# Kernel tuning notes

Measured on AMD Instinct MI355X. Metric: run time of the kernel, lower is better.

## Reference

```python
import jax, jax.numpy as jnp
import numpy as np

B, L, C, H = 8, 2048, 512, 8
HD = C // H
MLP_H = int(C * 4.0)
LN_EPS = 1e-5


def _dwconv(x, w, b, groups):
    # x: (B, C, L), w: (C, C//groups, 3), 'same' padding depthwise/grouped conv
    y = jax.lax.conv_general_dilated(
        x, w, window_strides=(1,), padding=((1, 1),),
        feature_group_count=groups,
        dimension_numbers=('NCH', 'OIH', 'NCH'))
    return y + b[None, :, None]


def _ln(x, g, b):
    mu = x.mean(-1, keepdims=True)
    var = ((x - mu) ** 2).mean(-1, keepdims=True)
    return (x - mu) * jax.lax.rsqrt(var + LN_EPS) * g + b


def setup_inputs() -> dict:
    key = jax.random.key(0)
    ks = jax.random.split(key, 32)
    s = 0.02
    d = {
        'x_q': jax.random.normal(ks[0], (B, L, C), jnp.float32),
        'x_kv': jax.random.normal(ks[1], (B, L, C), jnp.float32),
        'cpe1_w': jax.random.normal(ks[2], (C, 1, 3), jnp.float32) * s,
        'cpe1_b': jnp.zeros((C,), jnp.float32),
        'norm1_g': jnp.ones((C,), jnp.float32),
        'norm1_b': jnp.zeros((C,), jnp.float32),
        'in_w': jax.random.normal(ks[3], (C, C), jnp.float32) * s,
        'in_b': jnp.zeros((C,), jnp.float32),
        'act_w': jax.random.normal(ks[4], (C, C), jnp.float32) * s,
        'act_b': jnp.zeros((C,), jnp.float32),
        'dwc_w': jax.random.normal(ks[5], (C, 1, 3), jnp.float32) * s,
        'dwc_b': jnp.zeros((C,), jnp.float32),
        'q_w': jax.random.normal(ks[6], (C, C), jnp.float32) * s,
        'q_b': jnp.zeros((C,), jnp.float32),
        'kv_w': jax.random.normal(ks[7], (C, 2 * C), jnp.float32) * s,
        'kv_b': jnp.zeros((2 * C,), jnp.float32),
        'lepe_w': jax.random.normal(ks[8], (C, 1, 3), jnp.float32) * s,
        'lepe_b': jnp.zeros((C,), jnp.float32),
        'out_w': jax.random.normal(ks[9], (C, C), jnp.float32) * s,
        'out_b': jnp.zeros((C,), jnp.float32),
        'cpe2_w': jax.random.normal(ks[10], (C, 1, 3), jnp.float32) * s,
        'cpe2_b': jnp.zeros((C,), jnp.float32),
        'norm2_g': jnp.ones((C,), jnp.float32),
        'norm2_b': jnp.zeros((C,), jnp.float32),
        'fc1_w': jax.random.normal(ks[11], (C, MLP_H), jnp.float32) * s,
        'fc1_b': jnp.zeros((MLP_H,), jnp.float32),
        'fc2_w': jax.random.normal(ks[12], (MLP_H, C), jnp.float32) * s,
        'fc2_b': jnp.zeros((C,), jnp.float32),
    }
    return d


def _linear_attention(x_q, x_kv, q_w, q_b, kv_w, kv_b, lepe_w, lepe_b):
    b, n, c = x_kv.shape
    kv = x_kv @ kv_w + kv_b                       # (b, n, 2c)
    k, v = kv[..., :c], kv[..., c:]
    q = jax.nn.elu(x_q @ q_w + q_b) + 1.0
    k = jax.nn.elu(k) + 1.0
    # (b, h, n, d)
    q = q.reshape(b, n, H, HD).transpose(0, 2, 1, 3)
    k = k.reshape(b, n, H, HD).transpose(0, 2, 1, 3)
    v = v.reshape(b, n, H, HD).transpose(0, 2, 1, 3)
    k_mean = k.mean(axis=2)                       # (b, h, d)
    z = 1.0 / (jnp.einsum('bhnd,bhd->bhn', q, k_mean) + 1e-6)
    scale = n ** (-0.5)
    kv_mat = jnp.einsum('bhnd,bhne->bhde', k * scale, v * scale)  # (b,h,d,d)
    out = jnp.einsum('bhnd,bhde->bhne', q, kv_mat) * z[..., None]
    out = out.transpose(0, 2, 1, 3).reshape(b, n, c)
    v_flat = v.transpose(0, 2, 1, 3).reshape(b, n, c).transpose(0, 2, 1)  # (b,c,n)
    out = out + _dwconv(v_flat, lepe_w, lepe_b, groups=c).transpose(0, 2, 1)
    return out


def reference(x_q, x_kv, cpe1_w, cpe1_b, norm1_g, norm1_b, in_w, in_b, act_w,
              act_b, dwc_w, dwc_b, q_w, q_b, kv_w, kv_b, lepe_w, lepe_b,
              out_w, out_b, cpe2_w, cpe2_b, norm2_g, norm2_b, fc1_w, fc1_b,
              fc2_w, fc2_b):
    b, l, c = x_kv.shape
    x = x_kv + _dwconv(x_kv.transpose(0, 2, 1), cpe1_w, cpe1_b, c).transpose(0, 2, 1)
    shortcut = x
    x = _ln(x, norm1_g, norm1_b)
    act_res = jax.nn.silu(x @ act_w + act_b)
    # NOTE: torch uses .view(B, C, L): a reshape, not a transpose -- replicate faithfully
    xp = (x @ in_w + in_b).reshape(b, c, l)
    xp = jax.nn.silu(_dwconv(xp, dwc_w, dwc_b, c)).reshape(b, l, c)
    xa = _linear_attention(x_q, xp, q_w, q_b, kv_w, kv_b, lepe_w, lepe_b)
    x = shortcut + ((xa * act_res) @ out_w + out_b)
    x = x + _dwconv(x.transpose(0, 2, 1), cpe2_w, cpe2_b, c).transpose(0, 2, 1)
    h = _ln(x, norm2_g, norm2_b)
    h = jax.nn.gelu(h @ fc1_w + fc1_b, approximate=False) @ fc2_w + fc2_b
    return x + h
```

## Files before the change

### kernel.cpp

```cpp
#include <hip/hip_runtime.h>
#include <cmath>


typedef __bf16 bf16;
typedef __bf16 bf16x8 __attribute__((ext_vector_type(8)));
typedef __bf16 bf16x4 __attribute__((ext_vector_type(4)));
typedef float  f32x4  __attribute__((ext_vector_type(4)));

#define B_  8
#define L_  2048
#define C_  512
#define M_  (B_ * L_)

__device__ __forceinline__ float fastrcp(float x) { return __builtin_amdgcn_rcpf(x); }

__device__ __forceinline__ float siluf(float x)
{
    return x * fastrcp(1.f + __expf(-x));
}
__device__ __forceinline__ float elu1f(float x) { return x > 0.f ? x + 1.f : __expf(x); }

__device__ __forceinline__ float geluf(float x)
{
    const float z = fabsf(x) * 0.70710678118654752f;
    const float t = fastrcp(__builtin_fmaf(z, 0.47047f, 1.f));
    const float poly = t * (0.3480242f + t * (-0.0958798f + t * 0.7478556f));
    const float erfz = __builtin_fmaf(-poly, __expf(-z * z), 1.f);
    const float hx = 0.5f * x;
    return __builtin_fmaf(hx, __builtin_copysignf(erfz, x), hx);
}

__device__ __forceinline__ void load_lds16(const bf16* g, bf16* l)
{
    __builtin_amdgcn_global_load_lds(
        (const __attribute__((address_space(1))) void*)g,
        (__attribute__((address_space(3))) void*)l, 16, 0, 0);
}

__global__ __launch_bounds__(256) void zero_k(float* __restrict__ p, int n)
{
    int i = blockIdx.x * 256 + threadIdx.x;
    if (i < n) p[i] = 0.f;
}

__global__ __launch_bounds__(64) void ws_diag_k(float* __restrict__ out, float v)
{
    if (threadIdx.x == 0 && blockIdx.x == 0) out[0] = v;
}

__global__ __launch_bounds__(256) void f32_to_bf16_k(
    const float* __restrict__ in, bf16* __restrict__ out, int n4)
{
    int i = blockIdx.x * 256 + threadIdx.x;
    if (i >= n4) return;
    float4 v = ((const float4*)in)[i];
    bf16x4 o = { (bf16)v.x, (bf16)v.y, (bf16)v.z, (bf16)v.w };
    ((bf16x4*)out)[i] = o;
}

struct TJob  { const float* W; bf16* Wt; int K; int N; int blk0; };
struct TJobs { TJob j[7]; };

__global__ __launch_bounds__(256) void transpose_all_k(TJobs jobs)
{
    __shared__ float tile[32][33];
    const int bid = blockIdx.x;
    int ji = 0;
#pragma unroll
    for (int i = 1; i < 7; ++i) if (bid >= jobs.j[i].blk0) ji = i;
    const float* W  = jobs.j[ji].W;
    bf16*        Wt = jobs.j[ji].Wt;
    const int K = jobs.j[ji].K, N = jobs.j[ji].N;
    const int rel = bid - jobs.j[ji].blk0;
    const int nb = N >> 5;
    const int n0 = (rel % nb) * 32, k0 = (rel / nb) * 32;
    const int tx = threadIdx.x & 31, ty = threadIdx.x >> 5;
#pragma unroll
    for (int i = 0; i < 32; i += 8)
        tile[ty + i][tx] = W[(size_t)(k0 + ty + i) * N + n0 + tx];
    __syncthreads();
#pragma unroll
    for (int i = 0; i < 32; i += 8)
        Wt[(size_t)(n0 + ty + i) * K + k0 + tx] = (bf16)tile[tx][ty + i];
}

__global__ __launch_bounds__(256) void cpe_ln_k(
    const float* __restrict__ xin, const float* __restrict__ cw,
    const float* __restrict__ cb, const float* __restrict__ g,
    const float* __restrict__ bb, float* __restrict__ xres,
    bf16* __restrict__ xln)
{
    const int token = blockIdx.x;
    const int l = token & (L_ - 1);
    const int tid = threadIdx.x;
    const float* row = xin + (size_t)token * C_;
    float v[2]; float s = 0.f, s2 = 0.f;
#pragma unroll
    for (int i = 0; i < 2; ++i) {
        const int c = tid + i * 256;
        float x0 = row[c];
        float xm = (l > 0)      ? row[c - C_] : 0.f;
        float xp = (l < L_ - 1) ? row[c + C_] : 0.f;
        float t = x0 + xm * cw[3*c] + x0 * cw[3*c+1] + xp * cw[3*c+2] + cb[c];
        v[i] = t; s += t; s2 += t * t;
    }
#pragma unroll
    for (int off = 32; off; off >>= 1) { s += __shfl_down(s, off); s2 += __shfl_down(s2, off); }
    __shared__ float rs[4], rs2[4];
    if ((tid & 63) == 0) { rs[tid >> 6] = s; rs2[tid >> 6] = s2; }
    __syncthreads();
    s  = rs[0] + rs[1] + rs[2] + rs[3];
    s2 = rs2[0] + rs2[1] + rs2[2] + rs2[3];
    const float mu = s * (1.f / C_);
    const float rstd = rsqrtf(s2 * (1.f / C_) - mu * mu + 1e-5f);
    float* orow = xres + (size_t)token * C_;
    bf16*  lrow = xln  + (size_t)token * C_;
#pragma unroll
    for (int i = 0; i < 2; ++i) {
        const int c = tid + i * 256;
        orow[c] = v[i];
        lrow[c] = (bf16)((v[i] - mu) * rstd * g[c] + bb[c]);
    }
}

__global__ __launch_bounds__(256) void dwc_silu_k(
    const bf16* __restrict__ Y, const float* __restrict__ w,
    const float* __restrict__ b, bf16* __restrict__ xp)
{
    const size_t idx = (size_t)blockIdx.x * 256 + threadIdx.x;
    const int m = (int)(idx & (size_t)(L_ * C_ - 1));
    const int ch = m >> 11;
    const int pos = m & (L_ - 1);
    float x0 = (float)Y[idx];
    float xm = (pos > 0)      ? (float)Y[idx - 1] : 0.f;
    float xq = (pos < L_ - 1) ? (float)Y[idx + 1] : 0.f;
    float t = xm * w[3*ch] + x0 * w[3*ch+1] + xq * w[3*ch+2] + b[ch];
    xp[idx] = (bf16)siluf(t);
}

__global__ __launch_bounds__(256) void ksum_k(
    const bf16* __restrict__ kvbT, float* __restrict__ ksum)
{
    const int c = blockIdx.x;
    const int wave = threadIdx.x >> 6, lane = threadIdx.x & 63;
#pragma unroll
    for (int i = 0; i < 2; ++i) {
        const int b = wave + i * 4;
        const bf16* src = kvbT + (size_t)c * M_ + b * L_ + lane * 32;
        float s = 0.f;
#pragma unroll
        for (int u = 0; u < 4; ++u) {
            bf16x8 v = *(const bf16x8*)(src + u * 8);
#pragma unroll
            for (int j = 0; j < 8; ++j) s += (float)v[j];
        }
#pragma unroll
        for (int o = 32; o; o >>= 1) s += __shfl_down(s, o);
        if (lane == 0) ksum[b * C_ + c] = s;
    }
}

__global__ __launch_bounds__(256) void kvmat_mfma_k(
    const bf16* __restrict__ kvbT, float* __restrict__ kvpart)
{
    const int bh = blockIdx.x, b = bh >> 3, h = bh & 7;
    const int tid = threadIdx.x;
    const int wave = tid >> 6, lane = tid & 63;
    const int l16 = lane & 15, quad = lane >> 4;
    __shared__ bf16 As[64 * 72];
    __shared__ bf16 Bs[64 * 72];
    const int r = tid >> 2;
    const int cseg = (tid & 3) * 16;
    const size_t kRow = (size_t)(h * 64 + r) * M_;
    const size_t vRow = (size_t)(512 + h * 64 + r) * M_;

    f32x4 acc[4];
    const f32x4 z4 = { 0.f, 0.f, 0.f, 0.f };
#pragma unroll
    for (int ni = 0; ni < 4; ++ni) acc[ni] = z4;

    for (int it = 0; it < 8; ++it) {
        const size_t colBase = (size_t)b * L_ + blockIdx.y * 512 + it * 64;
        {
            const bf16* ga = kvbT + vRow + colBase + cseg;
            const bf16* gb = kvbT + kRow + colBase + cseg;
            *(uint4*)&As[r * 72 + cseg]     = *(const uint4*)ga;
            *(uint4*)&As[r * 72 + cseg + 8] = *(const uint4*)(ga + 8);
            *(uint4*)&Bs[r * 72 + cseg]     = *(const uint4*)gb;
            *(uint4*)&Bs[r * 72 + cseg + 8] = *(const uint4*)(gb + 8);
        }
        __syncthreads();
#pragma unroll
        for (int kk = 0; kk < 64; kk += 32) {
            bf16x8 af = *(const bf16x8*)(&As[(wave * 16 + l16) * 72 + kk + quad * 8]);
#pragma unroll
            for (int ni = 0; ni < 4; ++ni) {
                bf16x8 bfr = *(const bf16x8*)(&Bs[(ni * 16 + l16) * 72 + kk + quad * 8]);
                acc[ni] = __builtin_amdgcn_mfma_f32_16x16x32_bf16(af, bfr, acc[ni], 0, 0, 0);
            }
        }
        __syncthreads();
    }
    float* dst = kvpart + (size_t)blockIdx.y * 262144 + (size_t)bh * 4096;
#pragma unroll
    for (int ni = 0; ni < 4; ++ni)
#pragma unroll
        for (int rr = 0; rr < 4; ++rr)
            dst[(wave * 16 + quad * 4 + rr) * 64 + ni * 16 + l16] = acc[ni][rr];
}

__global__ __launch_bounds__(256) void kvconv_k(
    const float* __restrict__ p, bf16* __restrict__ out)
{
    int i = blockIdx.x * 256 + threadIdx.x;
    float s = p[i] + p[i + 262144] + p[i + 2 * 262144] + p[i + 3 * 262144];
    out[i] = (bf16)(s * (1.f / (float)L_));
}

__global__ __launch_bounds__(256) void attn_mfma_k(
    const bf16* __restrict__ q, const bf16* __restrict__ kvbT,
    const bf16* __restrict__ kvmatT, const float* __restrict__ ksum,
    const float* __restrict__ lw, const float* __restrict__ lb,
    const bf16* __restrict__ act_res, bf16* __restrict__ xa_mul)
{
    const int bh = blockIdx.x, b = bh >> 3, h = bh & 7;
    const int n0 = blockIdx.y * 64;
    const int tid = threadIdx.x;
    const int wave = tid >> 6, lane = tid & 63;
    const int l16 = lane & 15, quad = lane >> 4;

    __shared__ bf16 kvT[64 * 72];
    __shared__ bf16 kmS[64];

#pragma unroll
    for (int i = 0; i < 2; ++i) {
        const int idx = i * 256 + tid;
        const int row = idx >> 3, col = (idx & 7) * 8;
        *(bf16x8*)&kvT[row * 72 + col] =
            *(const bf16x8*)&kvmatT[(size_t)bh * 4096 + idx * 8];
    }
    if (tid < 64) kmS[tid] = (bf16)(ksum[b * C_ + h * 64 + tid] * (1.f / (float)L_));
    __syncthreads();

    const int tok = n0 + wave * 16;
    const bf16* qbase = q + ((size_t)b * L_ + tok) * C_ + h * 64;
    const bf16x8 af0 = *(const bf16x8*)(qbase + (size_t)l16 * C_ + quad * 8);
    const bf16x8 af1 = *(const bf16x8*)(qbase + (size_t)l16 * C_ + 32 + quad * 8);

    const bf16x8 z8 = { bf16(0.f), bf16(0.f), bf16(0.f), bf16(0.f),
                        bf16(0.f), bf16(0.f), bf16(0.f), bf16(0.f) };
    const bf16x8 km0 = *(const bf16x8*)&kmS[quad * 8];
    const bf16x8 km1 = *(const bf16x8*)&kmS[32 + quad * 8];
    const bf16x8 b20 = (l16 == 0) ? km0 : z8;
    const bf16x8 b21 = (l16 == 0) ? km1 : z8;
    f32x4 zd = { 0.f, 0.f, 0.f, 0.f };
    zd = __builtin_amdgcn_mfma_f32_16x16x32_bf16(af0, b20, zd, 0, 0, 0);
    zd = __builtin_amdgcn_mfma_f32_16x16x32_bf16(af1, b21, zd, 0, 0, 0);
    float zr[4];
#pragma unroll
    for (int r = 0; r < 4; ++r)
        zr[r] = fastrcp(__shfl(zd[r], (lane & 48)) + 1e-6f);

    f32x4 acc[4];
    const f32x4 zf4 = { 0.f, 0.f, 0.f, 0.f };
#pragma unroll
    for (int ni = 0; ni < 4; ++ni) acc[ni] = zf4;
#pragma unroll
    for (int ni = 0; ni < 4; ++ni) {
        const bf16x8 b0 = *(const bf16x8*)&kvT[(ni * 16 + l16) * 72 + quad * 8];
        const bf16x8 b1 = *(const bf16x8*)&kvT[(ni * 16 + l16) * 72 + 32 + quad * 8];
        acc[ni] = __builtin_amdgcn_mfma_f32_16x16x32_bf16(af0, b0, acc[ni], 0, 0, 0);
        acc[ni] = __builtin_amdgcn_mfma_f32_16x16x32_bf16(af1, b1, acc[ni], 0, 0, 0);
    }

#pragma unroll
    for (int ni = 0; ni < 4; ++ni) {
        const int e = ni * 16 + l16;
        const int c = h * 64 + e;
        const float w0 = lw[3*c], w1 = lw[3*c+1], w2 = lw[3*c+2], lbc = lb[c];
        const bf16* vrow = kvbT + (size_t)(512 + c) * M_ + b * L_;
#pragma unroll
        for (int r = 0; r < 4; ++r) {
            const int n = tok + quad * 4 + r;
            const float v0 = (float)vrow[n];
            const float vm = (n > 0)      ? (float)vrow[n - 1] : 0.f;
            const float vp = (n < L_ - 1) ? (float)vrow[n + 1] : 0.f;
            const float lepe = vm * w0 + v0 * w1 + vp * w2 + lbc;
            const float xa = acc[ni][r] * zr[r] + lepe;
            const size_t off = ((size_t)b * L_ + n) * C_ + c;
            xa_mul[off] = (bf16)(xa * (float)act_res[off]);
        }
    }
}

template <int EPI>
__global__ __launch_bounds__(256) void gemm_bt(
    const bf16* __restrict__ A, const bf16* __restrict__ Bt,
    const float* __restrict__ bias, const float* __restrict__ res,
    void* __restrict__ outp, void* __restrict__ outp2, int K, int N)
{
    __shared__ bf16 As[128 * 64];
    __shared__ bf16 Bs[128 * 64];
    const int tid = threadIdx.x;
    const int wave = tid >> 6, lane = tid & 63;
    const int wm = (wave & 1) * 64, wn = (wave >> 1) * 64;
    const int l16 = lane & 15, quad = lane >> 4;
    const size_t tileM = (size_t)blockIdx.x * 128;
    const size_t tileN = (size_t)blockIdx.y * 128;

    const int lrow = lane >> 3;
    const int lcol = (((lane & 7) ^ (lrow & 7))) * 8;
    const int swz  = l16 & 7;

    const f32x4 z4 = { 0.f, 0.f, 0.f, 0.f };
    f32x4 acc[4][4];
#pragma unroll
    for (int mi = 0; mi < 4; ++mi)
#pragma unroll
        for (int ni = 0; ni < 4; ++ni) acc[mi][ni] = z4;

    for (int k0 = 0; k0 < K; k0 += 64) {
#pragma unroll
        for (int it = 0; it < 4; ++it) {
            const int rg = it * 32 + wave * 8;
            load_lds16(A  + (tileM + rg + lrow) * (size_t)K + k0 + lcol, As + rg * 64);
            load_lds16(Bt + (tileN + rg + lrow) * (size_t)K + k0 + lcol, Bs + rg * 64);
        }
        __syncthreads();
#pragma unroll
        for (int kk = 0; kk < 64; kk += 32) {
            bf16x8 af[4], bfr[4];
#pragma unroll
            for (int mi = 0; mi < 4; ++mi)
                af[mi] = *(const bf16x8*)(&As[(wm + mi * 16 + l16) * 64
                                              + ((((kk >> 3) + quad) ^ swz) * 8)]);
#pragma unroll
            for (int ni = 0; ni < 4; ++ni)
                bfr[ni] = *(const bf16x8*)(&Bs[(wn + ni * 16 + l16) * 64
                                               + ((((kk >> 3) + quad) ^ swz) * 8)]);
#pragma unroll
            for (int mi = 0; mi < 4; ++mi)
#pragma unroll
                for (int ni = 0; ni < 4; ++ni)
                    acc[mi][ni] = __builtin_amdgcn_mfma_f32_16x16x32_bf16(
                        af[mi], bfr[ni], acc[mi][ni], 0, 0, 0);
        }
        __syncthreads();
    }

#pragma unroll
    for (int mi = 0; mi < 4; ++mi) {
#pragma unroll
        for (int ni = 0; ni < 4; ++ni) {
#pragma unroll
            for (int r = 0; r < 4; ++r) {
                const size_t row = tileM + wm + mi * 16 + quad * 4 + r;
                const int   col = (int)tileN + wn + ni * 16 + l16;
                float v = acc[mi][ni][r];
                const size_t oidx = row * (size_t)N + col;
                if (EPI == 2)      ((bf16*)outp)[oidx] = (bf16)elu1f(v + bias[col]);
                else if (EPI == 4) ((bf16*)outp)[oidx] = (bf16)geluf(v + bias[col]);
                else if (EPI == 5) ((float*)outp)[oidx] = v + bias[col] + res[oidx];
                else if (EPI == 7) {
                    v += bias[(int)row];
                    ((bf16*)outp)[oidx] = (bf16)((row < 512) ? elu1f(v) : v);
                } else if (EPI == 8) {
                    const size_t orow = row * (size_t)512;
                    if (col < 512) ((bf16*)outp )[orow + col]       = (bf16)siluf(v + bias[col]);
                    else           ((bf16*)outp2)[orow + col - 512] = (bf16)(v + res[col - 512]);
                }
            }
        }
    }
}

#define OFF_WT_ACTIN ((size_t)0)
#define OFF_WT_Q    ((size_t)1048576)
#define OFF_WT_KV   ((size_t)1572864)
#define OFF_WT_OUT  ((size_t)2621440)
#define OFF_WT_FC1  ((size_t)3145728)
#define OFF_WT_FC2  ((size_t)5242880)
#define OFF_XLN     ((size_t)7340032)
#define OFF_ACTRES  ((size_t)24117248)
#define OFF_Y       ((size_t)40894464)
#define OFF_XP      ((size_t)57671680)
#define OFF_KV      ((size_t)74448896)
#define OFF_KSUM    ((size_t)108003328)
#define OFF_XAMUL   ((size_t)109068288)
#define OFF_X3      ((size_t)24117248)
#define OFF_H1      ((size_t)57671680)
#define WS_REQUIRED ((size_t)125845504)

extern "C" void kernel_launch(void* const* d_in, const int* in_sizes, int n_in,
                              void* d_out, int out_size, void* d_ws, size_t ws_size,
                              hipStream_t stream)
{
    const float* x_q    = (const float*)d_in[0];
    const float* x_kv   = (const float*)d_in[1];
    const float* cpe1_w = (const float*)d_in[2];
    const float* cpe1_b = (const float*)d_in[3];
    const float* n1_g   = (const float*)d_in[4];
    const float* n1_b   = (const float*)d_in[5];
    const float* in_w   = (const float*)d_in[6];
    const float* in_b   = (const float*)d_in[7];
    const float* act_w  = (const float*)d_in[8];
    const float* act_b  = (const float*)d_in[9];
    const float* dwc_w  = (const float*)d_in[10];
    const float* dwc_b  = (const float*)d_in[11];
    const float* q_w    = (const float*)d_in[12];
    const float* q_b    = (const float*)d_in[13];
    const float* kv_w   = (const float*)d_in[14];
    const float* kv_b   = (const float*)d_in[15];
    const float* lepe_w = (const float*)d_in[16];
    const float* lepe_b = (const float*)d_in[17];
    const float* out_w  = (const float*)d_in[18];
    const float* out_b  = (const float*)d_in[19];
    const float* cpe2_w = (const float*)d_in[20];
    const float* cpe2_b = (const float*)d_in[21];
    const float* n2_g   = (const float*)d_in[22];
    const float* n2_b   = (const float*)d_in[23];
    const float* fc1_w  = (const float*)d_in[24];
    const float* fc1_b  = (const float*)d_in[25];
    const float* fc2_w  = (const float*)d_in[26];
    const float* fc2_b  = (const float*)d_in[27];

    float* outf = (float*)d_out;

    if (ws_size < WS_REQUIRED) {
        zero_k<<<(out_size + 255) / 256, 256, 0, stream>>>(outf, out_size);
        ws_diag_k<<<1, 64, 0, stream>>>(outf, (float)ws_size);
        return;
    }

    char* ws = (char*)d_ws;
    bf16*  wt_actin = (bf16*)(ws + OFF_WT_ACTIN);
    bf16*  wt_q   = (bf16*)(ws + OFF_WT_Q);
    bf16*  wt_kv  = (bf16*)(ws + OFF_WT_KV);
    bf16*  wt_out = (bf16*)(ws + OFF_WT_OUT);
    bf16*  wt_fc1 = (bf16*)(ws + OFF_WT_FC1);
    bf16*  wt_fc2 = (bf16*)(ws + OFF_WT_FC2);
    bf16*  xln    = (bf16*)(ws + OFF_XLN);
    bf16*  xqb    = (bf16*)(ws + OFF_XLN);
    bf16*  kvbf   = (bf16*)(ws + OFF_XLN);
    bf16*  hln    = (bf16*)(ws + OFF_XLN);
    bf16*  actres = (bf16*)(ws + OFF_ACTRES);
    bf16*  Y      = (bf16*)(ws + OFF_Y);
    bf16*  qb     = (bf16*)(ws + OFF_Y);
    bf16*  xp     = (bf16*)(ws + OFF_XP);
    float* kvpart = (float*)(ws + OFF_XP);
    bf16*  kvbT   = (bf16*)(ws + OFF_KV);
    float* ksum   = (float*)(ws + OFF_KSUM);
    bf16*  xamul  = (bf16*)(ws + OFF_XAMUL);
    float* x3     = (float*)(ws + OFF_X3);
    bf16*  h1     = (bf16*)(ws + OFF_H1);

    TJobs jobs;
    jobs.j[0] = { act_w, wt_actin,             512,  512,    0 };
    jobs.j[1] = { in_w,  wt_actin + 512 * 512, 512,  512,  256 };
    jobs.j[2] = { q_w,   wt_q,                 512,  512,  512 };
    jobs.j[3] = { kv_w,  wt_kv,                512, 1024,  768 };
    jobs.j[4] = { out_w, wt_out,               512,  512, 1280 };
    jobs.j[5] = { fc1_w, wt_fc1,               512, 2048, 1536 };
    jobs.j[6] = { fc2_w, wt_fc2,              2048,  512, 2560 };
    transpose_all_k<<<3584, 256, 0, stream>>>(jobs);

    cpe_ln_k<<<M_, 256, 0, stream>>>(x_kv, cpe1_w, cpe1_b, n1_g, n1_b, outf, xln);

    gemm_bt<8><<<dim3(128, 8), 256, 0, stream>>>(xln, wt_actin, act_b, in_b, actres, Y, 512, 1024);

    dwc_silu_k<<<32768, 256, 0, stream>>>(Y, dwc_w, dwc_b, xp);

    f32_to_bf16_k<<<8192, 256, 0, stream>>>(x_q, xqb, M_ * C_ / 4);
    gemm_bt<2><<<dim3(128, 4), 256, 0, stream>>>(xqb, wt_q, q_b, nullptr, qb, nullptr, 512, 512);

    gemm_bt<7><<<dim3(8, 128), 256, 0, stream>>>(wt_kv, xp, kv_b, nullptr, kvbT, nullptr, 512, M_);

    ksum_k<<<C_, 256, 0, stream>>>(kvbT, ksum);
    kvmat_mfma_k<<<dim3(64, 4), 256, 0, stream>>>(kvbT, kvpart);
    kvconv_k<<<1024, 256, 0, stream>>>(kvpart, kvbf);

    attn_mfma_k<<<dim3(64, 32), 256, 0, stream>>>(qb, kvbT, kvbf, ksum,
                                                  lepe_w, lepe_b, actres, xamul);

    gemm_bt<5><<<dim3(128, 4), 256, 0, stream>>>(xamul, wt_out, out_b, outf, outf, nullptr, 512, 512);

    cpe_ln_k<<<M_, 256, 0, stream>>>(outf, cpe2_w, cpe2_b, n2_g, n2_b, x3, hln);

    gemm_bt<4><<<dim3(128, 16), 256, 0, stream>>>(hln, wt_fc1, fc1_b, nullptr, h1, nullptr, 512, 2048);
    gemm_bt<5><<<dim3(128, 4),  256, 0, stream>>>(h1,  wt_fc2, fc2_b, x3, outf, nullptr, 2048, 512);

    (void)in_sizes; (void)n_in; (void)out_size; (void)ws_size;
}
```

Baseline: 493.4 us.

## Add 256x256-tile 8-wave GEMM with phased prefetch for wide GEMMs

Adds a new GEMM kernel using 256x256 output tiles, 512 threads (8 waves), double-buffered LDS, and a four-phase schedule that interleaves LDS reads, global prefetches and MFMA bursts with priority raises. It replaces the 128x128-style gemm_bt for the act/in, kv and fc1 GEMMs, aiming at more reuse per loaded tile and better overlap of loads with math. The cost is much more LDS per block (128 KB), more accumulator registers, and fewer blocks, which may hurt occupancy or leave CUs idle on the smaller grids.

```diff
diff --git a/kernel.cpp b/kernel.cpp
--- a/kernel.cpp
+++ b/kernel.cpp
@@ -356,6 +356,180 @@
             for (int r = 0; r < 4; ++r) {
                 const size_t row = tileM + wm + mi * 16 + quad * 4 + r;
                 const int   col = (int)tileN + wn + ni * 16 + l16;
+                float v = acc[mi][ni][r];
+                const size_t oidx = row * (size_t)N + col;
+                if (EPI == 2)      ((bf16*)outp)[oidx] = (bf16)elu1f(v + bias[col]);
+                else if (EPI == 4) ((bf16*)outp)[oidx] = (bf16)geluf(v + bias[col]);
+                else if (EPI == 5) ((float*)outp)[oidx] = v + bias[col] + res[oidx];
+                else if (EPI == 7) {
+                    v += bias[(int)row];
+                    ((bf16*)outp)[oidx] = (bf16)((row < 512) ? elu1f(v) : v);
+                } else if (EPI == 8) {
+                    const size_t orow = row * (size_t)512;
+                    if (col < 512) ((bf16*)outp )[orow + col]       = (bf16)siluf(v + bias[col]);
+                    else           ((bf16*)outp2)[orow + col - 512] = (bf16)(v + res[col - 512]);
+                }
+            }
+        }
+    }
+}
+
+template <int EPI>
+__global__ __launch_bounds__(512, 2) void gemm8(
+    const bf16* __restrict__ A, const bf16* __restrict__ Bt,
+    const float* __restrict__ bias, const float* __restrict__ res,
+    void* __restrict__ outp, void* __restrict__ outp2, int K, int N)
+{
+    __shared__ bf16 As[2][256 * 64];
+    __shared__ bf16 Bs[2][256 * 64];
+    const int tid  = threadIdx.x;
+    const int wave = tid >> 6, lane = tid & 63;
+    const int wrow = wave >> 2, wcol = wave & 3;
+    const int l16 = lane & 15, quad = lane >> 4;
+    const int lrow = lane >> 3;
+    const int lcol = ((lane & 7) ^ lrow) * 8;
+    const int swz  = l16 & 7;
+    const size_t tileM = (size_t)blockIdx.x * 256;
+    const size_t tileN = (size_t)blockIdx.y * 256;
+
+    const bf16* aBase = A  + (tileM + wave * 8 + lrow) * (size_t)K + lcol;
+    const bf16* bBase = Bt + (tileN + wave * 8 + lrow) * (size_t)K + lcol;
+    const int ldsRow0 = wave * 8;
+
+    f32x4 acc[8][4];
+    const f32x4 z4 = { 0.f, 0.f, 0.f, 0.f };
+#pragma unroll
+    for (int mi = 0; mi < 8; ++mi)
+#pragma unroll
+        for (int ni = 0; ni < 4; ++ni) acc[mi][ni] = z4;
+
+#pragma unroll
+    for (int j = 0; j < 4; ++j) {
+        load_lds16(aBase + (size_t)(j * 64) * K, &As[0][(j * 64 + ldsRow0) * 64]);
+        load_lds16(bBase + (size_t)(j * 64) * K, &Bs[0][(j * 64 + ldsRow0) * 64]);
+    }
+    asm volatile("s_waitcnt vmcnt(0)" ::: "memory");
+    __builtin_amdgcn_s_barrier();
+
+    const int T = K >> 6;
+    int cur = 0;
+    for (int t = 0; t < T; ++t) {
+        const int nxt = cur ^ 1;
+        const bool pf = (t + 1 < T);
+        const int kc = (t + 1) << 6;
+        const bf16* as = &As[cur][0];
+        const bf16* bs = &Bs[cur][0];
+        bf16x8 af[4][2], bfr[4][2];
+
+#pragma unroll
+        for (int j = 0; j < 4; ++j)
+#pragma unroll
+            for (int kh = 0; kh < 2; ++kh)
+                af[j][kh] = *(const bf16x8*)&as[(wrow * 128 + j * 16 + l16) * 64
+                                               + (((kh * 4 + quad) ^ swz) * 8)];
+#pragma unroll
+        for (int ni = 0; ni < 2; ++ni)
+#pragma unroll
+            for (int kh = 0; kh < 2; ++kh)
+                bfr[ni][kh] = *(const bf16x8*)&bs[(wcol * 64 + ni * 16 + l16) * 64
+                                                  + (((kh * 4 + quad) ^ swz) * 8)];
+        if (pf) {
+#pragma unroll
+            for (int j = 0; j < 2; ++j) {
+                load_lds16(aBase + (size_t)(j * 64) * K + kc, &As[nxt][(j * 64 + ldsRow0) * 64]);
+                load_lds16(bBase + (size_t)(j * 64) * K + kc, &Bs[nxt][(j * 64 + ldsRow0) * 64]);
+            }
+        }
+        __builtin_amdgcn_s_barrier();
+        asm volatile("s_waitcnt lgkmcnt(0)" ::: "memory");
+        __builtin_amdgcn_sched_barrier(0);
+        __builtin_amdgcn_s_setprio(1);
+#pragma unroll
+        for (int j = 0; j < 4; ++j)
+#pragma unroll
+            for (int ni = 0; ni < 2; ++ni)
+#pragma unroll
+                for (int kh = 0; kh < 2; ++kh)
+                    acc[j][ni] = __builtin_amdgcn_mfma_f32_16x16x32_bf16(
+                        af[j][kh], bfr[ni][kh], acc[j][ni], 0, 0, 0);
+        __builtin_amdgcn_s_setprio(0);
+        __builtin_amdgcn_s_barrier();
+
+#pragma unroll
+        for (int ni = 2; ni < 4; ++ni)
+#pragma unroll
+            for (int kh = 0; kh < 2; ++kh)
+                bfr[ni][kh] = *(const bf16x8*)&bs[(wcol * 64 + ni * 16 + l16) * 64
+                                                  + (((kh * 4 + quad) ^ swz) * 8)];
+        if (pf) {
+#pragma unroll
+            for (int j = 2; j < 4; ++j) {
+                load_lds16(aBase + (size_t)(j * 64) * K + kc, &As[nxt][(j * 64 + ldsRow0) * 64]);
+                load_lds16(bBase + (size_t)(j * 64) * K + kc, &Bs[nxt][(j * 64 + ldsRow0) * 64]);
+            }
+        }
+        __builtin_amdgcn_s_barrier();
+        asm volatile("s_waitcnt lgkmcnt(0)" ::: "memory");
+        __builtin_amdgcn_sched_barrier(0);
+        __builtin_amdgcn_s_setprio(1);
+#pragma unroll
+        for (int j = 0; j < 4; ++j)
+#pragma unroll
+            for (int ni = 2; ni < 4; ++ni)
+#pragma unroll
+                for (int kh = 0; kh < 2; ++kh)
+                    acc[j][ni] = __builtin_amdgcn_mfma_f32_16x16x32_bf16(
+                        af[j][kh], bfr[ni][kh], acc[j][ni], 0, 0, 0);
+        __builtin_amdgcn_s_setprio(0);
+        __builtin_amdgcn_s_barrier();
+
+#pragma unroll
+        for (int j = 0; j < 4; ++j)
+#pragma unroll
+            for (int kh = 0; kh < 2; ++kh)
+                af[j][kh] = *(const bf16x8*)&as[(wrow * 128 + 64 + j * 16 + l16) * 64
+                                               + (((kh * 4 + quad) ^ swz) * 8)];
+        __builtin_amdgcn_s_barrier();
+        asm volatile("s_waitcnt lgkmcnt(0)" ::: "memory");
+        __builtin_amdgcn_sched_barrier(0);
+        __builtin_amdgcn_s_setprio(1);
+#pragma unroll
+        for (int j = 0; j < 4; ++j)
+#pragma unroll
+            for (int ni = 0; ni < 2; ++ni)
+#pragma unroll
+                for (int kh = 0; kh < 2; ++kh)
+                    acc[4 + j][ni] = __builtin_amdgcn_mfma_f32_16x16x32_bf16(
+                        af[j][kh], bfr[ni][kh], acc[4 + j][ni], 0, 0, 0);
+        __builtin_amdgcn_s_setprio(0);
+        __builtin_amdgcn_s_barrier();
+
+        if (pf) asm volatile("s_waitcnt vmcnt(0)" ::: "memory");
+        __builtin_amdgcn_s_barrier();
+        __builtin_amdgcn_sched_barrier(0);
+        __builtin_amdgcn_s_setprio(1);
+#pragma unroll
+        for (int j = 0; j < 4; ++j)
+#pragma unroll
+            for (int ni = 2; ni < 4; ++ni)
+#pragma unroll
+                for (int kh = 0; kh < 2; ++kh)
+                    acc[4 + j][ni] = __builtin_amdgcn_mfma_f32_16x16x32_bf16(
+                        af[j][kh], bfr[ni][kh], acc[4 + j][ni], 0, 0, 0);
+        __builtin_amdgcn_s_setprio(0);
+        __builtin_amdgcn_s_barrier();
+
+        cur = nxt;
+    }
+
+#pragma unroll
+    for (int mi = 0; mi < 8; ++mi) {
+#pragma unroll
+        for (int ni = 0; ni < 4; ++ni) {
+#pragma unroll
+            for (int r = 0; r < 4; ++r) {
+                const size_t row = tileM + wrow * 128 + mi * 16 + quad * 4 + r;
+                const int   col = (int)tileN + wcol * 64 + ni * 16 + l16;
                 float v = acc[mi][ni][r];
                 const size_t oidx = row * (size_t)N + col;
                 if (EPI == 2)      ((bf16*)outp)[oidx] = (bf16)elu1f(v + bias[col]);
@@ -466,14 +640,14 @@
 
     cpe_ln_k<<<M_, 256, 0, stream>>>(x_kv, cpe1_w, cpe1_b, n1_g, n1_b, outf, xln);
 
-    gemm_bt<8><<<dim3(128, 8), 256, 0, stream>>>(xln, wt_actin, act_b, in_b, actres, Y, 512, 1024);
+    gemm8<8><<<dim3(64, 4), 512, 0, stream>>>(xln, wt_actin, act_b, in_b, actres, Y, 512, 1024);
 
     dwc_silu_k<<<32768, 256, 0, stream>>>(Y, dwc_w, dwc_b, xp);
 
     f32_to_bf16_k<<<8192, 256, 0, stream>>>(x_q, xqb, M_ * C_ / 4);
     gemm_bt<2><<<dim3(128, 4), 256, 0, stream>>>(xqb, wt_q, q_b, nullptr, qb, nullptr, 512, 512);
 
-    gemm_bt<7><<<dim3(8, 128), 256, 0, stream>>>(wt_kv, xp, kv_b, nullptr, kvbT, nullptr, 512, M_);
+    gemm8<7><<<dim3(4, 64), 512, 0, stream>>>(wt_kv, xp, kv_b, nullptr, kvbT, nullptr, 512, M_);
 
     ksum_k<<<C_, 256, 0, stream>>>(kvbT, ksum);
     kvmat_mfma_k<<<dim3(64, 4), 256, 0, stream>>>(kvbT, kvpart);
@@ -486,7 +660,7 @@
 
     cpe_ln_k<<<M_, 256, 0, stream>>>(outf, cpe2_w, cpe2_b, n2_g, n2_b, x3, hln);
 
-    gemm_bt<4><<<dim3(128, 16), 256, 0, stream>>>(hln, wt_fc1, fc1_b, nullptr, h1, nullptr, 512, 2048);
+    gemm8<4><<<dim3(64, 8), 512, 0, stream>>>(hln, wt_fc1, fc1_b, nullptr, h1, nullptr, 512, 2048);
     gemm_bt<5><<<dim3(128, 4),  256, 0, stream>>>(h1,  wt_fc2, fc2_b, x3, outf, nullptr, 2048, 512);
 
     (void)in_sizes; (void)n_in; (void)out_size; (void)ws_size;
```

Result: no change. 487.2 us (-1.3%).

## Add 256x256-tile 8-wave pipelined GEMM for act/in, kv and fc1 projections

Applied to the files above, without the earlier changes.

Introduces a new GEMM kernel with 512 threads and 256x256 output tiles. It double-buffers direct-to-LDS loads split into K-halves with swizzled layouts, and interleaves MFMA phases with barriers and s_setprio. The kernel replaces the 128-tile gemm_bt for the act/in, kv and fc1 projections, aiming for more data reuse per LDS load and overlap of global loads with matrix math. In exchange it uses far more LDS and registers per block and launches fewer blocks, which could leave CUs underused. The hand-tuned waitcnt counts could also be fragile.

```diff
diff --git a/kernel.cpp b/kernel.cpp
--- a/kernel.cpp
+++ b/kernel.cpp
@@ -356,6 +356,152 @@
             for (int r = 0; r < 4; ++r) {
                 const size_t row = tileM + wm + mi * 16 + quad * 4 + r;
                 const int   col = (int)tileN + wn + ni * 16 + l16;
+                float v = acc[mi][ni][r];
+                const size_t oidx = row * (size_t)N + col;
+                if (EPI == 2)      ((bf16*)outp)[oidx] = (bf16)elu1f(v + bias[col]);
+                else if (EPI == 4) ((bf16*)outp)[oidx] = (bf16)geluf(v + bias[col]);
+                else if (EPI == 5) ((float*)outp)[oidx] = v + bias[col] + res[oidx];
+                else if (EPI == 7) {
+                    v += bias[(int)row];
+                    ((bf16*)outp)[oidx] = (bf16)((row < 512) ? elu1f(v) : v);
+                } else if (EPI == 8) {
+                    const size_t orow = row * (size_t)512;
+                    if (col < 512) ((bf16*)outp )[orow + col]       = (bf16)siluf(v + bias[col]);
+                    else           ((bf16*)outp2)[orow + col - 512] = (bf16)(v + res[col - 512]);
+                }
+            }
+        }
+    }
+}
+
+template <int EPI>
+__global__ __launch_bounds__(512, 2) void gemm8(
+    const bf16* __restrict__ A, const bf16* __restrict__ Bt,
+    const float* __restrict__ bias, const float* __restrict__ res,
+    void* __restrict__ outp, void* __restrict__ outp2, int K, int N)
+{
+    __shared__ bf16 As[2][2][256 * 32];
+    __shared__ bf16 Bs[2][2][256 * 32];
+    const int tid  = threadIdx.x;
+    const int wave = tid >> 6, lane = tid & 63;
+    const int wrow = wave >> 2, wcol = wave & 3;
+    const int l16 = lane & 15, quad = lane >> 4;
+    const size_t tileM = (size_t)blockIdx.x * 256;
+    const size_t tileN = (size_t)blockIdx.y * 256;
+
+    const int srow   = lane >> 2;
+    const int schunk = ((lane & 3) ^ ((lane >> 3) & 3)) * 8;
+    const bf16* aSrc = A  + (tileM + wave * 32 + srow) * (size_t)K + schunk;
+    const bf16* bSrc = Bt + (tileN + wave * 32 + srow) * (size_t)K + schunk;
+
+    const int rperm = (quad ^ ((l16 >> 1) & 3)) * 8;
+
+    f32x4 acc[8][4];
+    const f32x4 z4 = { 0.f, 0.f, 0.f, 0.f };
+#pragma unroll
+    for (int mi = 0; mi < 8; ++mi)
+#pragma unroll
+        for (int ni = 0; ni < 4; ++ni) acc[mi][ni] = z4;
+
+#define STAGE(SRC, DST, buf, s, kh) do {                                        \
+    load_lds16(SRC + (size_t)(s) * 64 + (kh) * 32,                              \
+               &DST[buf][kh][(wave * 32) * 32]);                                \
+    load_lds16(SRC + (size_t)16 * K + (size_t)(s) * 64 + (kh) * 32,             \
+               &DST[buf][kh][(wave * 32 + 16) * 32]);                           \
+} while (0)
+#define LDA(m, buf, kh, mi)                                                     \
+    af[m] = *(const bf16x8*)&As[buf][kh][(wrow * 128 + (mi) * 16 + l16) * 32 + rperm]
+#define LDB(n, buf, kh)                                                         \
+    bfr[n] = *(const bf16x8*)&Bs[buf][kh][(wcol * 64 + (n) * 16 + l16) * 32 + rperm]
+#define MFMA_Q(mo)                                                              \
+    _Pragma("unroll") for (int m = 0; m < 4; ++m)                               \
+    _Pragma("unroll") for (int n = 0; n < 4; ++n)                               \
+        acc[(mo) + m][n] = __builtin_amdgcn_mfma_f32_16x16x32_bf16(             \
+            af[m], bfr[n], acc[(mo) + m][n], 0, 0, 0)
+#define PH_ENTER do { __builtin_amdgcn_s_barrier();                             \
+    asm volatile("s_waitcnt lgkmcnt(0)" ::: "memory");                          \
+    __builtin_amdgcn_sched_barrier(0);                                          \
+    __builtin_amdgcn_s_setprio(1); } while (0)
+#define PH_EXIT  do { __builtin_amdgcn_s_setprio(0);                            \
+    __builtin_amdgcn_s_barrier(); } while (0)
+
+    STAGE(aSrc, As, 0, 0, 0); STAGE(bSrc, Bs, 0, 0, 0);
+    STAGE(aSrc, As, 0, 0, 1); STAGE(bSrc, Bs, 0, 0, 1);
+    STAGE(aSrc, As, 1, 1, 0); STAGE(bSrc, Bs, 1, 1, 0);
+    asm volatile("s_waitcnt vmcnt(8)" ::: "memory");
+    __builtin_amdgcn_s_barrier();
+
+    const int NIT = K >> 7;
+    for (int it = 0; it < NIT; ++it) {
+        const bool lastI = (it == NIT - 1);
+        const int s1 = 2 * it + 1, s2 = 2 * it + 2, s3 = 2 * it + 3;
+        bf16x8 af[4], bfr[4];
+
+        LDA(0, 0, 0, 0); LDA(1, 0, 0, 1); LDA(2, 0, 0, 2); LDA(3, 0, 0, 3);
+        LDB(0, 0, 0);    LDB(1, 0, 0);    LDB(2, 0, 0);    LDB(3, 0, 0);
+        STAGE(aSrc, As, 1, s1, 1);
+        PH_ENTER; MFMA_Q(0); PH_EXIT;
+
+        LDA(0, 0, 0, 4); LDA(1, 0, 0, 5); LDA(2, 0, 0, 6); LDA(3, 0, 0, 7);
+        STAGE(bSrc, Bs, 1, s1, 1);
+        PH_ENTER; MFMA_Q(4);
+        __builtin_amdgcn_s_setprio(0);
+        asm volatile("s_waitcnt vmcnt(8)" ::: "memory");
+        __builtin_amdgcn_s_barrier();
+
+        LDA(0, 0, 1, 0); LDA(1, 0, 1, 1); LDA(2, 0, 1, 2); LDA(3, 0, 1, 3);
+        LDB(0, 0, 1);    LDB(1, 0, 1);    LDB(2, 0, 1);    LDB(3, 0, 1);
+        if (!lastI) STAGE(aSrc, As, 0, s2, 0);
+        PH_ENTER; MFMA_Q(0); PH_EXIT;
+
+        LDA(0, 0, 1, 4); LDA(1, 0, 1, 5); LDA(2, 0, 1, 6); LDA(3, 0, 1, 7);
+        if (!lastI) STAGE(bSrc, Bs, 0, s2, 0);
+        PH_ENTER; MFMA_Q(4);
+        __builtin_amdgcn_s_setprio(0);
+        if (!lastI) { asm volatile("s_waitcnt vmcnt(8)" ::: "memory"); }
+        else        { asm volatile("s_waitcnt vmcnt(4)" ::: "memory"); }
+        __builtin_amdgcn_s_barrier();
+
+        LDA(0, 1, 0, 0); LDA(1, 1, 0, 1); LDA(2, 1, 0, 2); LDA(3, 1, 0, 3);
+        LDB(0, 1, 0);    LDB(1, 1, 0);    LDB(2, 1, 0);    LDB(3, 1, 0);
+        if (!lastI) STAGE(aSrc, As, 0, s2, 1);
+        PH_ENTER; MFMA_Q(0); PH_EXIT;
+
+        LDA(0, 1, 0, 4); LDA(1, 1, 0, 5); LDA(2, 1, 0, 6); LDA(3, 1, 0, 7);
+        if (!lastI) STAGE(bSrc, Bs, 0, s2, 1);
+        PH_ENTER; MFMA_Q(4);
+        __builtin_amdgcn_s_setprio(0);
+        if (!lastI) { asm volatile("s_waitcnt vmcnt(8)" ::: "memory"); }
+        else        { asm volatile("s_waitcnt vmcnt(0)" ::: "memory"); }
+        __builtin_amdgcn_s_barrier();
+
+        LDA(0, 1, 1, 0); LDA(1, 1, 1, 1); LDA(2, 1, 1, 2); LDA(3, 1, 1, 3);
+        LDB(0, 1, 1);    LDB(1, 1, 1);    LDB(2, 1, 1);    LDB(3, 1, 1);
+        if (!lastI) STAGE(aSrc, As, 1, s3, 0);
+        PH_ENTER; MFMA_Q(0); PH_EXIT;
+
+        LDA(0, 1, 1, 4); LDA(1, 1, 1, 5); LDA(2, 1, 1, 6); LDA(3, 1, 1, 7);
+        if (!lastI) STAGE(bSrc, Bs, 1, s3, 0);
+        PH_ENTER; MFMA_Q(4);
+        __builtin_amdgcn_s_setprio(0);
+        if (!lastI) { asm volatile("s_waitcnt vmcnt(8)" ::: "memory"); }
+        __builtin_amdgcn_s_barrier();
+    }
+#undef STAGE
+#undef LDA
+#undef LDB
+#undef MFMA_Q
+#undef PH_ENTER
+#undef PH_EXIT
+
+#pragma unroll
+    for (int mi = 0; mi < 8; ++mi) {
+#pragma unroll
+        for (int ni = 0; ni < 4; ++ni) {
+#pragma unroll
+            for (int r = 0; r < 4; ++r) {
+                const size_t row = tileM + wrow * 128 + mi * 16 + quad * 4 + r;
+                const int   col = (int)tileN + wcol * 64 + ni * 16 + l16;
                 float v = acc[mi][ni][r];
                 const size_t oidx = row * (size_t)N + col;
                 if (EPI == 2)      ((bf16*)outp)[oidx] = (bf16)elu1f(v + bias[col]);
@@ -466,14 +612,14 @@
 
     cpe_ln_k<<<M_, 256, 0, stream>>>(x_kv, cpe1_w, cpe1_b, n1_g, n1_b, outf, xln);
 
-    gemm_bt<8><<<dim3(128, 8), 256, 0, stream>>>(xln, wt_actin, act_b, in_b, actres, Y, 512, 1024);
+    gemm8<8><<<dim3(64, 4), 512, 0, stream>>>(xln, wt_actin, act_b, in_b, actres, Y, 512, 1024);
 
     dwc_silu_k<<<32768, 256, 0, stream>>>(Y, dwc_w, dwc_b, xp);
 
     f32_to_bf16_k<<<8192, 256, 0, stream>>>(x_q, xqb, M_ * C_ / 4);
     gemm_bt<2><<<dim3(128, 4), 256, 0, stream>>>(xqb, wt_q, q_b, nullptr, qb, nullptr, 512, 512);
 
-    gemm_bt<7><<<dim3(8, 128), 256, 0, stream>>>(wt_kv, xp, kv_b, nullptr, kvbT, nullptr, 512, M_);
+    gemm8<7><<<dim3(4, 64), 512, 0, stream>>>(wt_kv, xp, kv_b, nullptr, kvbT, nullptr, 512, M_);
 
     ksum_k<<<C_, 256, 0, stream>>>(kvbT, ksum);
     kvmat_mfma_k<<<dim3(64, 4), 256, 0, stream>>>(kvbT, kvpart);
@@ -486,7 +632,7 @@
 
     cpe_ln_k<<<M_, 256, 0, stream>>>(outf, cpe2_w, cpe2_b, n2_g, n2_b, x3, hln);
 
-    gemm_bt<4><<<dim3(128, 16), 256, 0, stream>>>(hln, wt_fc1, fc1_b, nullptr, h1, nullptr, 512, 2048);
+    gemm8<4><<<dim3(64, 8), 512, 0, stream>>>(hln, wt_fc1, fc1_b, nullptr, h1, nullptr, 512, 2048);
     gemm_bt<5><<<dim3(128, 4),  256, 0, stream>>>(h1,  wt_fc2, fc2_b, x3, outf, nullptr, 2048, 512);
 
     (void)in_sizes; (void)n_in; (void)out_size; (void)ws_size;
```

Result: no change. 492.0 us (-0.3%).
